# Kernel optimization log

Hardware: AMD Instinct MI355X
Metric: run time of the kernel (lower is better)

## Reference

```python
import jax, jax.numpy as jnp
import numpy as np

N_NUM, N_CAT, CAT_W, N_ICD = 64, 32, 8, 128
BATCH = 131072


def setup_inputs() -> dict:
    key = jax.random.key(0)
    k1, k2, k3, k4, k5 = jax.random.split(key, 5)
    numerical_x = jax.random.normal(k1, (N_NUM, BATCH), dtype=jnp.float32)
    categorical_x = jax.random.uniform(k2, (N_CAT, BATCH, CAT_W), dtype=jnp.float32)
    icd_x = jax.random.normal(k3, (N_ICD, BATCH), dtype=jnp.float32)
    n_feature = N_NUM + N_CAT * CAT_W + N_ICD  # 448
    n_phenotype = N_NUM + N_CAT + N_ICD        # 224
    W = jax.random.normal(k4, (2, n_feature), dtype=jnp.float32)
    M = jax.random.normal(k5, (2, n_phenotype), dtype=jnp.float32)
    return {"numerical_x": numerical_x, "categorical_x": categorical_x,
            "icd_x": icd_x, "W": W, "M": M}


def reference(numerical_x, categorical_x, icd_x, W, M):
    # numerical_x: [n_num, B]; categorical_x: [n_cat, B, w]; icd_x: [n_icd, B]
    n_num = numerical_x.shape[0]
    n_cat, _, w = categorical_x.shape
    # W column layout matches the original sequential consumption order:
    W_num = W[:, :n_num]                                        # [2, n_num]
    W_cat = W[:, n_num:n_num + n_cat * w].reshape(2, n_cat, w)   # [2, n_cat, w]
    W_icd = W[:, n_num + n_cat * w:]                             # [2, n_icd]
    M_num = M[:, :n_num]
    M_cat = M[:, n_num:n_num + n_cat]
    M_icd = M[:, n_num + n_cat:]
    # per-feature: out_j = M[:, j, None] * tanh(W_block @ x_j.T); f = sum_j out_j
    f_num = jnp.einsum('cn,cnb->cb', M_num,
                       jnp.tanh(W_num[:, :, None] * numerical_x[None, :, :]))
    f_cat = jnp.einsum('cg,cgb->cb', M_cat,
                       jnp.tanh(jnp.einsum('cgw,gbw->cgb', W_cat, categorical_x)))
    f_icd = jnp.einsum('cn,cnb->cb', M_icd,
                       jnp.tanh(W_icd[:, :, None] * icd_x[None, :, :]))
    f = f_num + f_cat + f_icd                                    # [2, B]
    # prob = exp(f) / sum_over_classes(exp(f))  == softmax over axis 0
    return jax.nn.softmax(f, axis=0)
```

## Files before the change

kernel.cpp:

```cpp
#include <hip/hip_runtime.h>

#define N_NUM 64
#define N_CAT 32
#define CAT_W 8
#define N_ICD 128
#define BATCH 131072

#define WROW 448
#define MROW 224

__device__ __forceinline__ float fast_tanh(float x) {
    float e = __expf(2.0f * x);
    return 1.0f - 2.0f * __builtin_amdgcn_rcpf(e + 1.0f);
}

__global__ void __launch_bounds__(256, 4)
phenotype_softmax_kernel(const float* __restrict__ num_x,
                         const float* __restrict__ cat_x,
                         const float* __restrict__ icd_x,
                         const float* __restrict__ W,
                         const float* __restrict__ M,
                         float* __restrict__ out) {
    __shared__ float4 sNum[N_NUM];
    __shared__ float4 sIcd[N_ICD];
    __shared__ float4 sCatW[N_CAT][4];
    __shared__ float2 sCatM[N_CAT];
    __shared__ float2 sPart[4][128];

    const int t = threadIdx.x;

    if (t < N_NUM) {
        sNum[t] = make_float4(W[t], W[WROW + t], M[t], M[MROW + t]);
    }
    if (t < N_ICD) {
        sIcd[t] = make_float4(W[320 + t], W[WROW + 320 + t],
                              M[96 + t],  M[MROW + 96 + t]);
    }
    if (t < N_CAT * 4) {
        int g = t >> 2, q = t & 3, w = 2 * q;
        int base = 64 + g * 8 + w;
        sCatW[g][q] = make_float4(W[base],     W[WROW + base],
                                  W[base + 1], W[WROW + base + 1]);
    }
    if (t < N_CAT) {
        sCatM[t] = make_float2(M[64 + t], M[MROW + 64 + t]);
    }
    __syncthreads();

    const int wave = t >> 6;
    const int lane = t & 63;
    const int b0   = blockIdx.x * 128 + 2 * lane;

    float f0a = 0.0f, f1a = 0.0f;
    float f0b = 0.0f, f1b = 0.0f;

    const int n0 = wave * 16;
#pragma unroll
    for (int i = 0; i < 16; ++i) {
        int n = n0 + i;
        float2 x = *reinterpret_cast<const float2*>(num_x + (size_t)n * BATCH + b0);
        float4 c = sNum[n];
        f0a = fmaf(c.z, fast_tanh(c.x * x.x), f0a);
        f1a = fmaf(c.w, fast_tanh(c.y * x.x), f1a);
        f0b = fmaf(c.z, fast_tanh(c.x * x.y), f0b);
        f1b = fmaf(c.w, fast_tanh(c.y * x.y), f1b);
    }

    const int g0 = wave * 8;
#pragma unroll
    for (int i = 0; i < 8; ++i) {
        int g = g0 + i;
        const float4* vp = reinterpret_cast<const float4*>(cat_x + ((size_t)g * BATCH + b0) * CAT_W);
        float4 va0 = vp[0];
        float4 va1 = vp[1];
        float4 vb0 = vp[2];
        float4 vb1 = vp[3];
        float4 p0 = sCatW[g][0];
        float4 p1 = sCatW[g][1];
        float4 p2 = sCatW[g][2];
        float4 p3 = sCatW[g][3];
        float sa0, sa1, sb0, sb1;
        sa0 = va0.x * p0.x;             sa1 = va0.x * p0.y;
        sb0 = vb0.x * p0.x;             sb1 = vb0.x * p0.y;
        sa0 = fmaf(va0.y, p0.z, sa0);   sa1 = fmaf(va0.y, p0.w, sa1);
        sb0 = fmaf(vb0.y, p0.z, sb0);   sb1 = fmaf(vb0.y, p0.w, sb1);
        sa0 = fmaf(va0.z, p1.x, sa0);   sa1 = fmaf(va0.z, p1.y, sa1);
        sb0 = fmaf(vb0.z, p1.x, sb0);   sb1 = fmaf(vb0.z, p1.y, sb1);
        sa0 = fmaf(va0.w, p1.z, sa0);   sa1 = fmaf(va0.w, p1.w, sa1);
        sb0 = fmaf(vb0.w, p1.z, sb0);   sb1 = fmaf(vb0.w, p1.w, sb1);
        sa0 = fmaf(va1.x, p2.x, sa0);   sa1 = fmaf(va1.x, p2.y, sa1);
        sb0 = fmaf(vb1.x, p2.x, sb0);   sb1 = fmaf(vb1.x, p2.y, sb1);
        sa0 = fmaf(va1.y, p2.z, sa0);   sa1 = fmaf(va1.y, p2.w, sa1);
        sb0 = fmaf(vb1.y, p2.z, sb0);   sb1 = fmaf(vb1.y, p2.w, sb1);
        sa0 = fmaf(va1.z, p3.x, sa0);   sa1 = fmaf(va1.z, p3.y, sa1);
        sb0 = fmaf(vb1.z, p3.x, sb0);   sb1 = fmaf(vb1.z, p3.y, sb1);
        sa0 = fmaf(va1.w, p3.z, sa0);   sa1 = fmaf(va1.w, p3.w, sa1);
        sb0 = fmaf(vb1.w, p3.z, sb0);   sb1 = fmaf(vb1.w, p3.w, sb1);
        float2 m = sCatM[g];
        f0a = fmaf(m.x, fast_tanh(sa0), f0a);
        f1a = fmaf(m.y, fast_tanh(sa1), f1a);
        f0b = fmaf(m.x, fast_tanh(sb0), f0b);
        f1b = fmaf(m.y, fast_tanh(sb1), f1b);
    }

    const int m0 = wave * 32;
#pragma unroll
    for (int i = 0; i < 32; ++i) {
        int n = m0 + i;
        float2 x = *reinterpret_cast<const float2*>(icd_x + (size_t)n * BATCH + b0);
        float4 c = sIcd[n];
        f0a = fmaf(c.z, fast_tanh(c.x * x.x), f0a);
        f1a = fmaf(c.w, fast_tanh(c.y * x.x), f1a);
        f0b = fmaf(c.z, fast_tanh(c.x * x.y), f0b);
        f1b = fmaf(c.w, fast_tanh(c.y * x.y), f1b);
    }

    sPart[wave][2 * lane]     = make_float2(f0a, f1a);
    sPart[wave][2 * lane + 1] = make_float2(f0b, f1b);
    __syncthreads();

    if (t < 128) {
        float2 p0 = sPart[0][t];
        float2 p1 = sPart[1][t];
        float2 p2 = sPart[2][t];
        float2 p3 = sPart[3][t];
        float a0 = (p0.x + p1.x) + (p2.x + p3.x);
        float a1 = (p0.y + p1.y) + (p2.y + p3.y);
        float d  = a0 - a1;
        float e0 = __expf(-d);
        float e1 = __expf(d);
        int bb = blockIdx.x * 128 + t;
        out[bb]         = __builtin_amdgcn_rcpf(1.0f + e0);
        out[BATCH + bb] = __builtin_amdgcn_rcpf(1.0f + e1);
    }
}

extern "C" void kernel_launch(void* const* d_in, const int* in_sizes, int n_in,
                              void* d_out, int out_size, void* d_ws, size_t ws_size,
                              hipStream_t stream) {
    const float* num_x = (const float*)d_in[0];
    const float* cat_x = (const float*)d_in[1];
    const float* icd_x = (const float*)d_in[2];
    const float* W     = (const float*)d_in[3];
    const float* M     = (const float*)d_in[4];
    float* out = (float*)d_out;

    dim3 block(256);
    dim3 grid(BATCH / 128);
    phenotype_softmax_kernel<<<grid, block, 0, stream>>>(num_x, cat_x, icd_x, W, M, out);
}
```

Before: 45.00 us.

## Software-pipeline global loads across feature groups with double-buffered registers

Reorganizes the per-wave loops into explicit load and compute phases with register double buffers. Loads for the next categorical or ICD chunk are issued before computing the current one, which raises memory-level parallelism and hides latency. The cost is higher register pressure, which may reduce occupancy under launch_bounds(256,4) or cause spills.

```diff
diff --git a/kernel.cpp b/kernel.cpp
--- a/kernel.cpp
+++ b/kernel.cpp
@@ -55,65 +55,102 @@
     float f0b = 0.0f, f1b = 0.0f;
 
     const int n0 = wave * 16;
-#pragma unroll
-    for (int i = 0; i < 16; ++i) {
-        int n = n0 + i;
-        float2 x = *reinterpret_cast<const float2*>(num_x + (size_t)n * BATCH + b0);
-        float4 c = sNum[n];
-        f0a = fmaf(c.z, fast_tanh(c.x * x.x), f0a);
-        f1a = fmaf(c.w, fast_tanh(c.y * x.x), f1a);
-        f0b = fmaf(c.z, fast_tanh(c.x * x.y), f0b);
-        f1b = fmaf(c.w, fast_tanh(c.y * x.y), f1b);
+    const int g0 = wave * 8;
+    const int m0 = wave * 32;
+
+    const float* numP = num_x + (size_t)n0 * BATCH + b0;
+    const float* icdP = icd_x + (size_t)m0 * BATCH + b0;
+    const float4* catP = reinterpret_cast<const float4*>(cat_x) + ((size_t)g0 * BATCH + b0) * 2;
+    const size_t CATG = (size_t)BATCH * 2;
+
+#define NUM_LOAD()                                                             \
+    _Pragma("unroll")                                                          \
+    for (int i = 0; i < 16; ++i)                                               \
+        xn[i] = *reinterpret_cast<const float2*>(numP + (size_t)i * BATCH);
+
+#define NUM_COMP()                                                             \
+    _Pragma("unroll")                                                          \
+    for (int i = 0; i < 16; ++i) {                                             \
+        float4 c = sNum[n0 + i];                                               \
+        f0a = fmaf(c.z, fast_tanh(c.x * xn[i].x), f0a);                        \
+        f1a = fmaf(c.w, fast_tanh(c.y * xn[i].x), f1a);                        \
+        f0b = fmaf(c.z, fast_tanh(c.x * xn[i].y), f0b);                        \
+        f1b = fmaf(c.w, fast_tanh(c.y * xn[i].y), f1b);                        \
     }
 
-    const int g0 = wave * 8;
-#pragma unroll
-    for (int i = 0; i < 8; ++i) {
-        int g = g0 + i;
-        const float4* vp = reinterpret_cast<const float4*>(cat_x + ((size_t)g * BATCH + b0) * CAT_W);
-        float4 va0 = vp[0];
-        float4 va1 = vp[1];
-        float4 vb0 = vp[2];
-        float4 vb1 = vp[3];
-        float4 p0 = sCatW[g][0];
-        float4 p1 = sCatW[g][1];
-        float4 p2 = sCatW[g][2];
-        float4 p3 = sCatW[g][3];
-        float sa0, sa1, sb0, sb1;
-        sa0 = va0.x * p0.x;             sa1 = va0.x * p0.y;
-        sb0 = vb0.x * p0.x;             sb1 = vb0.x * p0.y;
-        sa0 = fmaf(va0.y, p0.z, sa0);   sa1 = fmaf(va0.y, p0.w, sa1);
-        sb0 = fmaf(vb0.y, p0.z, sb0);   sb1 = fmaf(vb0.y, p0.w, sb1);
-        sa0 = fmaf(va0.z, p1.x, sa0);   sa1 = fmaf(va0.z, p1.y, sa1);
-        sb0 = fmaf(vb0.z, p1.x, sb0);   sb1 = fmaf(vb0.z, p1.y, sb1);
-        sa0 = fmaf(va0.w, p1.z, sa0);   sa1 = fmaf(va0.w, p1.w, sa1);
-        sb0 = fmaf(vb0.w, p1.z, sb0);   sb1 = fmaf(vb0.w, p1.w, sb1);
-        sa0 = fmaf(va1.x, p2.x, sa0);   sa1 = fmaf(va1.x, p2.y, sa1);
-        sb0 = fmaf(vb1.x, p2.x, sb0);   sb1 = fmaf(vb1.x, p2.y, sb1);
-        sa0 = fmaf(va1.y, p2.z, sa0);   sa1 = fmaf(va1.y, p2.w, sa1);
-        sb0 = fmaf(vb1.y, p2.z, sb0);   sb1 = fmaf(vb1.y, p2.w, sb1);
-        sa0 = fmaf(va1.z, p3.x, sa0);   sa1 = fmaf(va1.z, p3.y, sa1);
-        sb0 = fmaf(vb1.z, p3.x, sb0);   sb1 = fmaf(vb1.z, p3.y, sb1);
-        sa0 = fmaf(va1.w, p3.z, sa0);   sa1 = fmaf(va1.w, p3.w, sa1);
-        sb0 = fmaf(vb1.w, p3.z, sb0);   sb1 = fmaf(vb1.w, p3.w, sb1);
-        float2 m = sCatM[g];
-        f0a = fmaf(m.x, fast_tanh(sa0), f0a);
-        f1a = fmaf(m.y, fast_tanh(sa1), f1a);
-        f0b = fmaf(m.x, fast_tanh(sb0), f0b);
-        f1b = fmaf(m.y, fast_tanh(sb1), f1b);
+#define CAT_LOAD(buf, gg)                                                      \
+    _Pragma("unroll")                                                          \
+    for (int j = 0; j < 2; ++j) {                                              \
+        const float4* vp = catP + (size_t)((gg) + j) * CATG;                   \
+        buf[j][0] = vp[0]; buf[j][1] = vp[1];                                  \
+        buf[j][2] = vp[2]; buf[j][3] = vp[3];                                  \
     }
 
-    const int m0 = wave * 32;
-#pragma unroll
-    for (int i = 0; i < 32; ++i) {
-        int n = m0 + i;
-        float2 x = *reinterpret_cast<const float2*>(icd_x + (size_t)n * BATCH + b0);
-        float4 c = sIcd[n];
-        f0a = fmaf(c.z, fast_tanh(c.x * x.x), f0a);
-        f1a = fmaf(c.w, fast_tanh(c.y * x.x), f1a);
-        f0b = fmaf(c.z, fast_tanh(c.x * x.y), f0b);
-        f1b = fmaf(c.w, fast_tanh(c.y * x.y), f1b);
+#define CAT_COMP(buf, gg)                                                      \
+    _Pragma("unroll")                                                          \
+    for (int j = 0; j < 2; ++j) {                                              \
+        int g = g0 + (gg) + j;                                                 \
+        float4 va0 = buf[j][0], va1 = buf[j][1];                               \
+        float4 vb0 = buf[j][2], vb1 = buf[j][3];                               \
+        float4 p0 = sCatW[g][0], p1 = sCatW[g][1];                             \
+        float4 p2 = sCatW[g][2], p3 = sCatW[g][3];                             \
+        float sa0, sa1, sb0, sb1;                                              \
+        sa0 = va0.x * p0.x;             sa1 = va0.x * p0.y;                    \
+        sb0 = vb0.x * p0.x;             sb1 = vb0.x * p0.y;                    \
+        sa0 = fmaf(va0.y, p0.z, sa0);   sa1 = fmaf(va0.y, p0.w, sa1);          \
+        sb0 = fmaf(vb0.y, p0.z, sb0);   sb1 = fmaf(vb0.y, p0.w, sb1);          \
+        sa0 = fmaf(va0.z, p1.x, sa0);   sa1 = fmaf(va0.z, p1.y, sa1);          \
+        sb0 = fmaf(vb0.z, p1.x, sb0);   sb1 = fmaf(vb0.z, p1.y, sb1);          \
+        sa0 = fmaf(va0.w, p1.z, sa0);   sa1 = fmaf(va0.w, p1.w, sa1);          \
+        sb0 = fmaf(vb0.w, p1.z, sb0);   sb1 = fmaf(vb0.w, p1.w, sb1);          \
+        sa0 = fmaf(va1.x, p2.x, sa0);   sa1 = fmaf(va1.x, p2.y, sa1);          \
+        sb0 = fmaf(vb1.x, p2.x, sb0);   sb1 = fmaf(vb1.x, p2.y, sb1);          \
+        sa0 = fmaf(va1.y, p2.z, sa0);   sa1 = fmaf(va1.y, p2.w, sa1);          \
+        sb0 = fmaf(vb1.y, p2.z, sb0);   sb1 = fmaf(vb1.y, p2.w, sb1);          \
+        sa0 = fmaf(va1.z, p3.x, sa0);   sa1 = fmaf(va1.z, p3.y, sa1);          \
+        sb0 = fmaf(vb1.z, p3.x, sb0);   sb1 = fmaf(vb1.z, p3.y, sb1);          \
+        sa0 = fmaf(va1.w, p3.z, sa0);   sa1 = fmaf(va1.w, p3.w, sa1);          \
+        sb0 = fmaf(vb1.w, p3.z, sb0);   sb1 = fmaf(vb1.w, p3.w, sb1);          \
+        float2 m = sCatM[g];                                                   \
+        f0a = fmaf(m.x, fast_tanh(sa0), f0a);                                  \
+        f1a = fmaf(m.y, fast_tanh(sa1), f1a);                                  \
+        f0b = fmaf(m.x, fast_tanh(sb0), f0b);                                  \
+        f1b = fmaf(m.y, fast_tanh(sb1), f1b);                                  \
     }
+
+#define ICD_LOAD(buf, ff)                                                      \
+    _Pragma("unroll")                                                          \
+    for (int i = 0; i < 16; ++i)                                               \
+        buf[i] = *reinterpret_cast<const float2*>(icdP + (size_t)((ff) + i) * BATCH);
+
+#define ICD_COMP(buf, ff)                                                      \
+    _Pragma("unroll")                                                          \
+    for (int i = 0; i < 16; ++i) {                                             \
+        float4 c = sIcd[m0 + (ff) + i];                                        \
+        f0a = fmaf(c.z, fast_tanh(c.x * buf[i].x), f0a);                       \
+        f1a = fmaf(c.w, fast_tanh(c.y * buf[i].x), f1a);                       \
+        f0b = fmaf(c.z, fast_tanh(c.x * buf[i].y), f0b);                       \
+        f1b = fmaf(c.w, fast_tanh(c.y * buf[i].y), f1b);                       \
+    }
+
+    float2 xn[16];
+    float4 cA[2][4], cB[2][4];
+    float2 iA[16], iB[16];
+
+    NUM_LOAD();
+    CAT_LOAD(cA, 0);
+    NUM_COMP();
+    CAT_LOAD(cB, 2);
+    CAT_COMP(cA, 0);
+    CAT_LOAD(cA, 4);
+    CAT_COMP(cB, 2);
+    CAT_LOAD(cB, 6);
+    CAT_COMP(cA, 4);
+    ICD_LOAD(iA, 0);
+    CAT_COMP(cB, 6);
+    ICD_LOAD(iB, 16);
+    ICD_COMP(iA, 0);
+    ICD_COMP(iB, 16);
 
     sPart[wave][2 * lane]     = make_float2(f0a, f1a);
     sPart[wave][2 * lane + 1] = make_float2(f0b, f1b);
```

After: 48.10 us. 1.07x slower.
